# Optimization experiments

Hardware: AMD Instinct MI355X
Metric: run time of the kernel (lower is better)

## Reference

```python
import jax, jax.numpy as jnp
import numpy as np

D = 1024   # hidden_size
H = 16     # n_head
K = 64     # head_size
B = 4
T = 1024
LAYER_ID = 12
NUM_LAYERS = 24
D_MIX = 32
D_DECAY = 64


def setup_inputs() -> dict:
    key = jax.random.key(0)
    ks = jax.random.split(key, 12)
    r01 = LAYER_ID / (NUM_LAYERS - 1)          # ratio_0_to_1
    r10 = 1.0 - LAYER_ID / NUM_LAYERS          # ratio_1_to_almost0
    ddd = jnp.arange(D, dtype=jnp.float32) / D
    maa = lambda p: (1.0 - ddd ** p).reshape(1, 1, D)
    inp = {}
    inp['x'] = jax.random.normal(ks[0], (B, T, D), jnp.float32)
    inp['time_maa_x'] = maa(r10)
    inp['time_maa_w'] = maa(r10)
    inp['time_maa_k'] = maa(r10)
    inp['time_maa_v'] = (1.0 - (ddd ** r10 + 0.3 * r01)).reshape(1, 1, D)
    inp['time_maa_r'] = maa(0.5 * r10)
    inp['time_maa_g'] = maa(0.5 * r10)
    # torch inits time_maa_w1 to zeros (trivial); use small uniform like w2 for a non-degenerate test
    inp['time_maa_w1'] = jax.random.uniform(ks[1], (D, D_MIX * 5), jnp.float32, -0.01, 0.01)
    inp['time_maa_w2'] = jax.random.uniform(ks[2], (5, D_MIX, D), jnp.float32, -0.01, 0.01)
    n = jnp.arange(D, dtype=jnp.float32)
    inp['time_decay'] = (-6.0 + 5.0 * (n / (D - 1)) ** (0.7 + 1.3 * r01)).reshape(1, 1, D)
    inp['time_decay_w1'] = jax.random.uniform(ks[3], (D, D_DECAY), jnp.float32, -0.01, 0.01)
    inp['time_decay_w2'] = jax.random.uniform(ks[4], (D_DECAY, D), jnp.float32, -0.01, 0.01)
    for nm, kk in zip(['W_r', 'W_k', 'W_v', 'W_g', 'W_o'], ks[5:10]):
        inp[nm] = jax.random.normal(kk, (D, D), jnp.float32) * 0.02
    inp['ln_w'] = jnp.ones((D,), jnp.float32)
    inp['ln_b'] = jnp.zeros((D,), jnp.float32)
    return inp


def _bidir_shift(x):
    # (x[i-1] + x[i+1]) / 2 with zero padding at the boundaries
    left = jnp.pad(x[:, :-1, :], ((0, 0), (1, 0), (0, 0)))
    right = jnp.pad(x[:, 1:, :], ((0, 0), (0, 1), (0, 0)))
    return 0.5 * (left + right)


def _lion_attention(r, k, v, w):
    # r,k,v,w: (B,H,T,Khd), w = -exp(decay) <= 0
    Tn = r.shape[2]
    cs = jnp.cumsum(w, axis=2)
    cs_b = cs - w
    shift_f = cs[:, :, Tn // 2:Tn // 2 + 1, :]
    shift_b = cs_b[:, :, Tn // 2:Tn // 2 + 1, :]
    cf = jnp.clip(cs - shift_f, -60.0, 60.0)
    cb = jnp.clip(cs_b - shift_b, -60.0, 60.0)
    # A_fwd = tril(Q*e^{cf} @ (K*e^{-cf})^T); A_bwd = triu(Q*e^{-cb} @ (K*e^{cb})^T, 1)
    A_f = jnp.einsum('bhik,bhjk->bhij', r * jnp.exp(cf), k * jnp.exp(-cf))
    A_b = jnp.einsum('bhik,bhjk->bhij', r * jnp.exp(-cb), k * jnp.exp(cb))
    idx = jnp.arange(Tn)
    lower = idx[:, None] >= idx[None, :]   # tril incl. diagonal
    A = jnp.where(lower, A_f, A_b)         # == tril(A_f) + triu(A_b, 1)
    return jnp.einsum('bhij,bhjk->bhik', A, v)


def reference(x, time_maa_x, time_maa_w, time_maa_k, time_maa_v, time_maa_r, time_maa_g,
              time_maa_w1, time_maa_w2, time_decay, time_decay_w1, time_decay_w2,
              W_r, W_k, W_v, W_g, W_o, ln_w, ln_b):
    Bn, Tn, Dn = x.shape
    Hh, Kk = H, Dn // H
    dxprev = _bidir_shift(x) - x
    # data-dependent token-shift mixing coefficients (LoRA-style)
    xxx = jnp.tanh((x + dxprev * time_maa_x) @ time_maa_w1)          # (B,T,5*32)
    mm = jnp.einsum('btfm,fmd->fbtd', xxx.reshape(Bn, Tn, 5, D_MIX), time_maa_w2)
    mw, mk, mv, mr, mg = mm[0], mm[1], mm[2], mm[3], mm[4]
    xw = x + dxprev * (time_maa_w + mw)
    xk = x + dxprev * (time_maa_k + mk)
    xv = x + dxprev * (time_maa_v + mv)
    xr = x + dxprev * (time_maa_r + mr)
    xg = x + dxprev * (time_maa_g + mg)
    r = xr @ W_r.T
    k = xk @ W_k.T
    v = xv @ W_v.T
    g = jax.nn.silu(xg @ W_g.T)
    w = time_decay + jnp.tanh(xw @ time_decay_w1) @ time_decay_w2   # (B,T,D)
    to_h = lambda t: t.reshape(Bn, Tn, Hh, Kk).transpose(0, 2, 1, 3)
    y = _lion_attention(to_h(r), to_h(k), to_h(v), -jnp.exp(to_h(w)))
    y = y.transpose(0, 2, 1, 3).reshape(Bn * Tn, Dn)
    # GroupNorm(n_head groups, eps = 1e-5 * head_size_divisor^2)
    eps = 1e-5 * 64.0
    yg = y.reshape(Bn * Tn, Hh, Kk)
    mu = jnp.mean(yg, axis=-1, keepdims=True)
    var = jnp.var(yg, axis=-1, keepdims=True)
    yn = ((yg - mu) * jax.lax.rsqrt(var + eps)).reshape(Bn * Tn, Dn) * ln_w + ln_b
    y = yn.reshape(Bn, Tn, Dn)
    return (y * g) @ W_o.T
```

## Files before the change

kernel.cpp:

```cpp
#include <hip/hip_runtime.h>
#include <math.h>

#define NB 4
#define TT 1024
#define DD 1024
#define NTOK 4096
#define ND (NTOK*DD)

typedef __attribute__((ext_vector_type(8))) short bh8;
typedef __attribute__((ext_vector_type(4))) float fx4;

__device__ __forceinline__ unsigned short f2bf(float f) {
    unsigned int b = __float_as_uint(f);
    b += 0x7fffu + ((b >> 16) & 1u);
    return (unsigned short)(b >> 16);
}

__device__ __forceinline__ unsigned pkbf(float a, float b) {
#if __has_builtin(__builtin_amdgcn_cvt_pk_bf16_f32)
    auto r = __builtin_amdgcn_cvt_pk_bf16_f32(a, b);
    unsigned u;
    __builtin_memcpy(&u, &r, 4);
    return u;
#else
    return ((unsigned)f2bf(b) << 16) | f2bf(a);
#endif
}

#define GLD16(gp, lp) __builtin_amdgcn_global_load_lds( \
    (__attribute__((address_space(1))) void*)(gp), \
    (__attribute__((address_space(3))) void*)(lp), 16, 0, 0)

#define BARF() do { __builtin_amdgcn_s_barrier(); asm volatile("" ::: "memory"); } while (0)

__global__ __launch_bounds__(256) void k_prep(const float* __restrict__ W_r, const float* __restrict__ W_k,
                                              const float* __restrict__ W_v, const float* __restrict__ W_g,
                                              const float* __restrict__ W_o,
                                              const float* __restrict__ w1, const float* __restrict__ dw1,
                                              const float* __restrict__ w2,
                                              unsigned short* __restrict__ Wrb, unsigned short* __restrict__ Wkb,
                                              unsigned short* __restrict__ Wvb, unsigned short* __restrict__ Wgb,
                                              unsigned short* __restrict__ Wob,
                                              unsigned short* __restrict__ w1T, unsigned short* __restrict__ dw1T,
                                              unsigned short* __restrict__ w2T16) {
    int y = blockIdx.y, bx = blockIdx.x, tid = threadIdx.x;
    if (y < 5) {
        if (bx >= 512) return;
        const float* s = (y == 0) ? W_r : (y == 1) ? W_k : (y == 2) ? W_v : (y == 3) ? W_g : W_o;
        unsigned short* d = (y == 0) ? Wrb : (y == 1) ? Wkb : (y == 2) ? Wvb : (y == 3) ? Wgb : Wob;
        int i = (bx * 256 + tid) * 8;
        float4 a = *(const float4*)(s + i);
        float4 b = *(const float4*)(s + i + 4);
        uint4 o;
        o.x = pkbf(a.x, a.y);
        o.y = pkbf(a.z, a.w);
        o.z = pkbf(b.x, b.y);
        o.w = pkbf(b.z, b.w);
        *(uint4*)(d + i) = o;
    } else if (y == 5) {
        int o = bx * 256 + tid;
        int r = o & 1023, c = o >> 10;
        w1T[o] = f2bf(w1[r * 160 + c]);
    } else {
        if (bx < 256) {
            int o = bx * 256 + tid;
            int r = o & 1023, c = o >> 10;
            dw1T[o] = f2bf(dw1[r * 64 + c]);
        } else if (bx < 276) {
            int wi = bx - 256;
            int f = wi >> 2;
            int d = (wi & 3) * 256 + tid;
#pragma unroll 8
            for (int m = 0; m < 32; m++)
                w2T16[(size_t)(f * 1024 + d) * 32 + m] = f2bf(w2[(size_t)(f * 32 + m) * 1024 + d]);
        }
    }
}

__global__ __launch_bounds__(256) void k_mixx(const float* __restrict__ x,
                                              const float* __restrict__ maa_x,
                                              unsigned short* __restrict__ xmix16) {
    int base = (blockIdx.x * 256 + threadIdx.x) * 4;
    int t = (base >> 10) & 1023;
    int d = base & 1023;
    float4 xv = *(const float4*)(x + base);
    float4 xm = (t > 0)    ? *(const float4*)(x + base - 1024) : make_float4(0, 0, 0, 0);
    float4 xp = (t < 1023) ? *(const float4*)(x + base + 1024) : make_float4(0, 0, 0, 0);
    float4 ma = *(const float4*)(maa_x + d);
    uint2 o;
    float a0 = xv.x + (0.5f * (xm.x + xp.x) - xv.x) * ma.x;
    float a1 = xv.y + (0.5f * (xm.y + xp.y) - xv.y) * ma.y;
    float a2 = xv.z + (0.5f * (xm.z + xp.z) - xv.z) * ma.z;
    float a3 = xv.w + (0.5f * (xm.w + xp.w) - xv.w) * ma.w;
    o.x = pkbf(a0, a1);
    o.y = pkbf(a2, a3);
    *(uint2*)(xmix16 + base) = o;
}

__global__ __launch_bounds__(64) void k_xxx2(const unsigned short* __restrict__ xmix16,
                                             const unsigned short* __restrict__ w1T,
                                             unsigned short* __restrict__ xxx16) {
    int lane = threadIdx.x;
    int l15 = lane & 15, qd = lane >> 4;
    int m0 = blockIdx.x * 16;
    fx4 acc[10];
#pragma unroll
    for (int nt = 0; nt < 10; nt++)
#pragma unroll
        for (int r = 0; r < 4; r++) acc[nt][r] = 0.f;
#pragma unroll 2
    for (int kb = 0; kb < 1024; kb += 32) {
        bh8 af = *(const bh8*)(xmix16 + (size_t)(m0 + l15) * 1024 + kb + qd * 8);
#pragma unroll
        for (int nt = 0; nt < 10; nt++) {
            bh8 bf = *(const bh8*)(w1T + (size_t)(nt * 16 + l15) * 1024 + kb + qd * 8);
            acc[nt] = __builtin_amdgcn_mfma_f32_16x16x32_bf16(af, bf, acc[nt], 0, 0, 0);
        }
    }
#pragma unroll
    for (int nt = 0; nt < 10; nt++)
#pragma unroll
        for (int r = 0; r < 4; r++)
            xxx16[(size_t)(m0 + qd * 4 + r) * 160 + nt * 16 + l15] = f2bf(tanhf(acc[nt][r]));
}

__global__ __launch_bounds__(256, 2) void k_mmix(const float* __restrict__ x,
                                                 const unsigned short* __restrict__ xxx16,
                                                 const unsigned short* __restrict__ w2T16,
                                                 const float* __restrict__ maa_w,
                                                 const float* __restrict__ maa_k,
                                                 const float* __restrict__ maa_v,
                                                 const float* __restrict__ maa_r,
                                                 const float* __restrict__ maa_g,
                                                 unsigned short* __restrict__ xw16,
                                                 unsigned short* __restrict__ xk16,
                                                 unsigned short* __restrict__ xv16,
                                                 unsigned short* __restrict__ xr16,
                                                 unsigned short* __restrict__ xg16) {
    int tid = threadIdx.x;
    int w = tid >> 6, lane = tid & 63, l15 = lane & 15, qd = lane >> 4;
    int n0 = blockIdx.x * 64;
    int m0w = blockIdx.y * 128 + w * 32;
    const float* maap[5] = {maa_w, maa_k, maa_v, maa_r, maa_g};
    unsigned short* outp[5] = {xw16, xk16, xv16, xr16, xg16};
    float xin[8][4], dxv[8][4];
#pragma unroll
    for (int mi = 0; mi < 2; mi++)
#pragma unroll
        for (int r = 0; r < 4; r++) {
            int tok = m0w + mi * 16 + qd * 4 + r;
            int t = tok & 1023;
#pragma unroll
            for (int ni = 0; ni < 4; ni++) {
                int d = n0 + ni * 16 + l15;
                size_t idx = (size_t)tok * 1024 + d;
                float xv = x[idx];
                float xm1 = (t > 0)    ? x[idx - 1024] : 0.f;
                float xp1 = (t < 1023) ? x[idx + 1024] : 0.f;
                xin[mi * 4 + r][ni] = xv;
                dxv[mi * 4 + r][ni] = 0.5f * (xm1 + xp1) - xv;
            }
        }
#pragma unroll
    for (int f = 0; f < 5; f++) {
        bh8 af[2], bf[4];
#pragma unroll
        for (int mi = 0; mi < 2; mi++)
            af[mi] = *(const bh8*)(xxx16 + (size_t)(m0w + mi * 16 + l15) * 160 + f * 32 + qd * 8);
#pragma unroll
        for (int ni = 0; ni < 4; ni++)
            bf[ni] = *(const bh8*)(w2T16 + (size_t)(f * 1024 + n0 + ni * 16 + l15) * 32 + qd * 8);
        fx4 acc[2][4];
#pragma unroll
        for (int mi = 0; mi < 2; mi++)
#pragma unroll
            for (int ni = 0; ni < 4; ni++) {
#pragma unroll
                for (int r = 0; r < 4; r++) acc[mi][ni][r] = 0.f;
                acc[mi][ni] = __builtin_amdgcn_mfma_f32_16x16x32_bf16(af[mi], bf[ni], acc[mi][ni], 0, 0, 0);
            }
        const float* maa = maap[f];
        unsigned short* op = outp[f];
#pragma unroll
        for (int ni = 0; ni < 4; ni++) {
            float mv = maa[n0 + ni * 16 + l15];
#pragma unroll
            for (int mi = 0; mi < 2; mi++)
#pragma unroll
                for (int r = 0; r < 4; r++) {
                    float o = xin[mi * 4 + r][ni] + dxv[mi * 4 + r][ni] * (mv + acc[mi][ni][r]);
                    op[(size_t)(m0w + mi * 16 + qd * 4 + r) * 1024 + n0 + ni * 16 + l15] = f2bf(o);
                }
        }
    }
}

__global__ __launch_bounds__(64) void k_dec1m(const unsigned short* __restrict__ xw16,
                                              const unsigned short* __restrict__ dw1T,
                                              float* __restrict__ dech) {
    int lane = threadIdx.x;
    int l15 = lane & 15, qd = lane >> 4;
    int m0 = blockIdx.x * 16;
    fx4 acc[4];
#pragma unroll
    for (int nt = 0; nt < 4; nt++)
#pragma unroll
        for (int r = 0; r < 4; r++) acc[nt][r] = 0.f;
#pragma unroll 2
    for (int kb = 0; kb < 1024; kb += 32) {
        bh8 af = *(const bh8*)(xw16 + (size_t)(m0 + l15) * 1024 + kb + qd * 8);
#pragma unroll
        for (int nt = 0; nt < 4; nt++) {
            bh8 bf = *(const bh8*)(dw1T + (size_t)(nt * 16 + l15) * 1024 + kb + qd * 8);
            acc[nt] = __builtin_amdgcn_mfma_f32_16x16x32_bf16(af, bf, acc[nt], 0, 0, 0);
        }
    }
#pragma unroll
    for (int nt = 0; nt < 4; nt++)
#pragma unroll
        for (int r = 0; r < 4; r++)
            dech[(size_t)(m0 + qd * 4 + r) * 64 + nt * 16 + l15] = tanhf(acc[nt][r]);
}

__global__ __launch_bounds__(256) void k_dec2(const float* __restrict__ dech,
                                              const float* __restrict__ dw2,
                                              const float* __restrict__ tdec,
                                              float* __restrict__ ew) {
    __shared__ float hl[8][64];
    int tid = threadIdx.x;
    int tok0 = blockIdx.x * 8;
    {
        int l = tid;        hl[l >> 6][l & 63] = dech[tok0 * 64 + l];
        l = tid + 256;      hl[l >> 6][l & 63] = dech[tok0 * 64 + l];
    }
    __syncthreads();
#pragma unroll 1
    for (int c = 0; c < 4; c++) {
        int d = c * 256 + tid;
        float acc[8] = {};
#pragma unroll 8
        for (int j = 0; j < 64; j++) {
            float wv = dw2[j * 1024 + d];
#pragma unroll
            for (int g = 0; g < 8; g++) acc[g] = fmaf(hl[g][j], wv, acc[g]);
        }
        float td = tdec[d];
#pragma unroll
        for (int g = 0; g < 8; g++) ew[(tok0 + g) * 1024 + d] = -expf(td + acc[g]);
    }
}

__global__ __launch_bounds__(64) void k_scan1(const float* __restrict__ ew, float* __restrict__ segsum) {
    int bx = blockIdx.x;
    int b = bx >> 9, seg = (bx >> 4) & 31, dch = bx & 15;
    int d = dch * 64 + threadIdx.x;
    size_t base = ((size_t)(b * 1024 + seg * 32)) * 1024 + d;
    float s = 0.f;
#pragma unroll 8
    for (int t = 0; t < 32; t++) s += ew[base + (size_t)t * 1024];
    segsum[(b * 32 + seg) * 1024 + d] = s;
}

__global__ __launch_bounds__(64) void k_scan3(const float* __restrict__ ew, const float* __restrict__ segsum,
                                              float* __restrict__ cf, float* __restrict__ cb) {
    int bx = blockIdx.x;
    int b = bx >> 9, seg = (bx >> 4) & 31, dch = bx & 15;
    int d = dch * 64 + threadIdx.x;
    float run = 0.f, pre = 0.f, off16 = 0.f;
#pragma unroll
    for (int s = 0; s < 32; s++) {
        float tv = segsum[(b * 32 + s) * 1024 + d];
        if (s == seg) pre = run;
        if (s == 16) off16 = run;
        run += tv;
    }
    float e512 = ew[((size_t)(b * 1024 + 512)) * 1024 + d];
    float sb = off16;
    float sf = off16 + e512;
    float cum = pre;
    size_t base = ((size_t)(b * 1024 + seg * 32)) * 1024 + d;
#pragma unroll 4
    for (int t = 0; t < 32; t++) {
        float prev = cum;
        cum += ew[base + (size_t)t * 1024];
        cf[base + (size_t)t * 1024] = fminf(fmaxf(cum - sf, -60.f), 60.f);
        cb[base + (size_t)t * 1024] = fminf(fmaxf(prev - sb, -60.f), 60.f);
    }
}

template<int NW, int BNv>
__device__ __forceinline__ void gemm_v5(const unsigned short* __restrict__ A,
                                        const unsigned short* __restrict__ W,
                                        int m0, int n0, int mode,
                                        float* __restrict__ Cf,
                                        unsigned short* __restrict__ O1,
                                        unsigned short* __restrict__ O2,
                                        const float* __restrict__ cfp,
                                        const float* __restrict__ cbp,
                                        char* smem) {
    constexpr int AR = 128 / NW;
    constexpr int AG = AR / 16;
    constexpr int BR = BNv / NW;
    constexpr int BG = BR / 16;
    constexpr int LPW = AG + BG;
    constexpr int SLOT = (128 + BNv) * 64;
    constexpr int WNC = BNv / 64;

    int tid = threadIdx.x;
    int lane = tid & 63, w = tid >> 6;
    int l15 = lane & 15, qd = lane >> 4;
    int wm = w / WNC, wn = w % WNC;
    int lr = lane >> 2, lb = lane & 3;
    int gblk = lb ^ ((lr >> 1) & 3);
    const unsigned short* aSrc = A + (size_t)(m0 + w * AR + lr) * 1024 + gblk * 8;
    const unsigned short* bSrc = W + (size_t)(n0 + w * BR + lr) * 1024 + gblk * 8;
    int rc = (qd ^ ((l15 >> 1) & 3)) * 8;
    int arow = (wm * 64 + l15) * 32 + rc;
    int brow = (wn * 64 + l15) * 32 + rc;

    auto stage = [&](int off, int kbv) {
        unsigned short* _sa = (unsigned short*)(smem + off);
        unsigned short* _sb = _sa + 128 * 32;
#pragma unroll
        for (int i = 0; i < AG; ++i)
            GLD16(aSrc + kbv + (size_t)i * 16 * 1024, _sa + (w * AR + i * 16) * 32);
#pragma unroll
        for (int i = 0; i < BG; ++i)
            GLD16(bSrc + kbv + (size_t)i * 16 * 1024, _sb + (w * BR + i * 16) * 32);
    };

    fx4 acc[4][4];
#pragma unroll
    for (int mt = 0; mt < 4; mt++)
#pragma unroll
        for (int nt = 0; nt < 4; nt++)
#pragma unroll
            for (int r = 0; r < 4; r++) acc[mt][nt][r] = 0.f;

    stage(0, 0);
    stage(SLOT, 32);
    if constexpr (LPW == 3) asm volatile("s_waitcnt vmcnt(3)" ::: "memory");
    else                    asm volatile("s_waitcnt vmcnt(4)" ::: "memory");
    BARF();

    int oc = 0, on = SLOT, o2 = 2 * SLOT;
#pragma unroll 1
    for (int t = 0; t < 32; ++t) {
        if (t < 30) stage(o2, (t + 2) * 32);
        const unsigned short* cA = (const unsigned short*)(smem + oc);
        const unsigned short* cB = cA + 128 * 32;
        bh8 a[4], b[4];
#pragma unroll
        for (int mt = 0; mt < 4; ++mt) a[mt] = *(const bh8*)(cA + arow + mt * 512);
#pragma unroll
        for (int nt = 0; nt < 4; ++nt) b[nt] = *(const bh8*)(cB + brow + nt * 512);
        __builtin_amdgcn_s_setprio(1);
#pragma unroll
        for (int nt = 0; nt < 4; ++nt)
#pragma unroll
            for (int mt = 0; mt < 4; ++mt)
                acc[mt][nt] = __builtin_amdgcn_mfma_f32_16x16x32_bf16(a[mt], b[nt], acc[mt][nt], 0, 0, 0);
        __builtin_amdgcn_s_setprio(0);
        asm volatile("s_waitcnt lgkmcnt(0)" ::: "memory");
        if (t < 30) {
            if constexpr (LPW == 3) asm volatile("s_waitcnt vmcnt(3)" ::: "memory");
            else                    asm volatile("s_waitcnt vmcnt(4)" ::: "memory");
        } else if (t == 30) {
            asm volatile("s_waitcnt vmcnt(0)" ::: "memory");
        }
        BARF();
        int tmp = oc; oc = on; on = o2; o2 = tmp;
    }

    int mb = m0 + wm * 64, nb = n0 + wn * 64;
    if (mode <= 1) {
#pragma unroll
        for (int mt = 0; mt < 4; mt++)
#pragma unroll
            for (int nt = 0; nt < 4; nt++)
#pragma unroll
                for (int r = 0; r < 4; r++) {
                    float v = acc[mt][nt][r];
                    if (mode == 1) v = v / (1.f + __expf(-v));
                    Cf[(size_t)(mb + mt * 16 + qd * 4 + r) * 1024 + nb + nt * 16 + l15] = v;
                }
    } else if (mode <= 3) {
        float s1 = (mode == 2) ? 1.f : -1.f;
#pragma unroll
        for (int mt = 0; mt < 4; mt++)
#pragma unroll
            for (int nt = 0; nt < 4; nt++)
#pragma unroll
                for (int r = 0; r < 4; r++) {
                    size_t idx = (size_t)(mb + mt * 16 + qd * 4 + r) * 1024 + nb + nt * 16 + l15;
                    float v = acc[mt][nt][r];
                    O1[idx] = f2bf(v * __expf(s1 * cfp[idx]));
                    O2[idx] = f2bf(v * __expf(-s1 * cbp[idx]));
                }
    } else {
        unsigned short* T = (unsigned short*)smem;
        int bq = m0 >> 10, t0 = m0 & 1023;
#pragma unroll
        for (int mt = 0; mt < 4; mt++)
#pragma unroll
            for (int nt = 0; nt < 4; nt++) {
                int dl = wn * 64 + nt * 16 + l15;
                int tl = wm * 64 + mt * 16 + qd * 4;
                uint2 pk2;
                pk2.x = pkbf(acc[mt][nt][0], acc[mt][nt][1]);
                pk2.y = pkbf(acc[mt][nt][2], acc[mt][nt][3]);
                *(uint2*)(T + dl * 136 + tl) = pk2;
            }
        asm volatile("s_waitcnt lgkmcnt(0)" ::: "memory");
        BARF();
#pragma unroll
        for (int p = 0; p < 8; ++p) {
            int idx = p * (NW * 64) + tid;
            int dd = idx >> 4, u = idx & 15;
            uint4 vv = *(const uint4*)(T + dd * 136 + u * 8);
            *(uint4*)(O1 + (size_t)(bq * 1024 + n0 + dd) * 1024 + t0 + u * 8) = vv;
        }
    }
}

__global__ __launch_bounds__(512, 4) void k_qkvg(const unsigned short* __restrict__ xr16,
                                                 const unsigned short* __restrict__ xk16,
                                                 const unsigned short* __restrict__ xv16,
                                                 const unsigned short* __restrict__ xg16,
                                                 const unsigned short* __restrict__ Wrb,
                                                 const unsigned short* __restrict__ Wkb,
                                                 const unsigned short* __restrict__ Wvb,
                                                 const unsigned short* __restrict__ Wgb,
                                                 unsigned short* __restrict__ qf, unsigned short* __restrict__ qb,
                                                 unsigned short* __restrict__ kf, unsigned short* __restrict__ kb,
                                                 unsigned short* __restrict__ vvt,
                                                 float* __restrict__ gg,
                                                 const float* __restrict__ cf, const float* __restrict__ cb) {
    __shared__ __align__(16) char smem[73728];
    int flat = blockIdx.x;
    int wkid = (flat & 7) * 64 + (flat >> 3);
    int gy = wkid >> 7;
    int rem = wkid & 127;
    int m0 = (rem >> 2) * 128, n0 = (rem & 3) * 256;
    const unsigned short* Ap = (gy == 0) ? xr16 : (gy == 1) ? xk16 : (gy == 2) ? xv16 : xg16;
    const unsigned short* Wp = (gy == 0) ? Wrb : (gy == 1) ? Wkb : (gy == 2) ? Wvb : Wgb;
    int mode = (gy == 0) ? 2 : (gy == 1) ? 3 : (gy == 2) ? 4 : 1;
    unsigned short* o1 = (gy == 0) ? qf : (gy == 1) ? kf : (gy == 2) ? vvt : nullptr;
    unsigned short* o2 = (gy == 0) ? qb : (gy == 1) ? kb : nullptr;
    float* cfo = (gy == 3) ? gg : nullptr;
    gemm_v5<8, 256>(Ap, Wp, m0, n0, mode, cfo, o1, o2, cf, cb, smem);
}

__global__ __launch_bounds__(256, 3) void k_gemmo(const unsigned short* __restrict__ z16,
                                                  const unsigned short* __restrict__ Wob,
                                                  float* __restrict__ out) {
    __shared__ __align__(16) char smem[49152];
    int flat = blockIdx.x;
    int wkid = (flat & 7) * 32 + (flat >> 3);
    int m0 = (wkid >> 3) * 128, n0 = (wkid & 7) * 128;
    gemm_v5<4, 128>(z16, Wob, m0, n0, 0, out, nullptr, nullptr, nullptr, nullptr, smem);
}

__global__ __launch_bounds__(256, 2) void k_attn(const unsigned short* __restrict__ qf,
                                                 const unsigned short* __restrict__ qb,
                                                 const unsigned short* __restrict__ kf,
                                                 const unsigned short* __restrict__ kb,
                                                 const unsigned short* __restrict__ vvt,
                                                 float* __restrict__ y) {
    __shared__ __align__(16) char smem[32768];
    unsigned short* sK = (unsigned short*)smem;
    unsigned short* sV = (unsigned short*)(smem + 16384);
    int tid = threadIdx.x;
    int w = tid >> 6, lane = tid & 63, l15 = lane & 15, qd = lane >> 4;
    int bid = blockIdx.x;
    int bh = (bid & 7) + ((bid >> 6) << 3);
    int ib = (bid >> 3) & 7;
    int b = bh >> 4, h = bh & 15;
    int i0w = ib * 128 + w * 32;
    int bt0 = b * 1024;
    const unsigned short* vrow = vvt + (size_t)(b * 1024 + h * 64 + w * 16 + l15) * 1024 + qd * 8;
    int fmax = (i0w + 31) >> 6;
    int bmin = i0w >> 6;
    int srcA = l15 + ((lane & 16) << 1);
    int srcB = srcA + 16;
    fx4 yacc[4][2];
#pragma unroll
    for (int mt = 0; mt < 4; mt++)
#pragma unroll
        for (int nt = 0; nt < 2; nt++)
#pragma unroll
            for (int r = 0; r < 4; r++) yacc[mt][nt][r] = 0.f;

    for (int phase = 0; phase < 2; phase++) {
        const unsigned short* Q = phase ? qb : qf;
        const unsigned short* K = phase ? kb : kf;
        bh8 qfr[2][2];
#pragma unroll
        for (int nt = 0; nt < 2; nt++)
#pragma unroll
            for (int ks = 0; ks < 2; ks++)
                qfr[nt][ks] = *(const bh8*)(Q + (size_t)(bt0 + i0w + nt * 16 + l15) * 1024
                                              + h * 64 + ks * 32 + qd * 8);
        int jlo = phase == 0 ? 0 : 2 * ib;
        int jhi = phase == 0 ? 2 * ib + 1 : 15;
        const unsigned short* krow = K + (size_t)(bt0 + w * 16 + l15) * 1024 + h * 64 + qd * 8;
        for (int jt2 = jlo; jt2 <= jhi; jt2 += 2) {
            __syncthreads();
#pragma unroll
            for (int u = 0; u < 2; ++u) {
                size_t jb = (size_t)(jt2 + u) * 64;
                GLD16(krow + jb * 1024,        sK + u * 4096 + w * 512);
                GLD16(krow + jb * 1024 + 32,   sK + u * 4096 + 2048 + w * 512);
                GLD16(vrow + jb,               sV + u * 4096 + w * 512);
                GLD16(vrow + jb + 32,          sV + u * 4096 + 2048 + w * 512);
            }
            __syncthreads();
#pragma unroll
            for (int u = 0; u < 2; ++u) {
                int jt = jt2 + u;
                int jb = jt * 64;
                const unsigned short* bK = sK + u * 4096;
                const unsigned short* bV = sV + u * 4096;
                bool active = (phase == 0) ? (jt <= fmax) : (jt >= bmin);
                if (!active) continue;
                bool needmask = (phase == 0) ? (jb + 63 > i0w) : (i0w + 31 >= jb);
                bh8 kc[8];
#pragma unroll
                for (int fi = 0; fi < 8; fi++)
                    kc[fi] = *(const bh8*)(bK + fi * 512 + lane * 8);
                fx4 sacc[4][2];
#pragma unroll
                for (int mt = 0; mt < 4; mt++)
#pragma unroll
                    for (int nt = 0; nt < 2; nt++)
#pragma unroll
                        for (int r = 0; r < 4; r++) sacc[mt][nt][r] = 0.f;
#pragma unroll
                for (int ks = 0; ks < 2; ks++)
#pragma unroll
                    for (int mt = 0; mt < 4; mt++)
#pragma unroll
                        for (int nt = 0; nt < 2; nt++)
                            sacc[mt][nt] = __builtin_amdgcn_mfma_f32_16x16x32_bf16(kc[ks * 4 + mt], qfr[nt][ks], sacc[mt][nt], 0, 0, 0);
                uint2 pk[4][2];
#pragma unroll
                for (int mt = 0; mt < 4; mt++)
#pragma unroll
                    for (int nt = 0; nt < 2; nt++) {
                        fx4 s = sacc[mt][nt];
                        if (needmask) {
                            int ii = i0w + nt * 16 + l15;
                            int jj0 = jb + mt * 16 + qd * 4;
#pragma unroll
                            for (int r = 0; r < 4; r++) {
                                bool keep = (phase == 0) ? (ii >= jj0 + r) : (ii < jj0 + r);
                                if (!keep) s[r] = 0.f;
                            }
                        }
                        pk[mt][nt].x = pkbf(s[0], s[1]);
                        pk[mt][nt].y = pkbf(s[2], s[3]);
                    }
                bh8 vc[8];
#pragma unroll
                for (int fi = 0; fi < 8; fi++)
                    vc[fi] = *(const bh8*)(bV + fi * 512 + lane * 8);
#pragma unroll
                for (int ks2 = 0; ks2 < 2; ks2++) {
#pragma unroll
                    for (int nt = 0; nt < 2; nt++) {
                        int lox  = __shfl((int)pk[2 * ks2][nt].x,     srcA);
                        int hix  = __shfl((int)pk[2 * ks2 + 1][nt].x, srcA);
                        int loy  = __shfl((int)pk[2 * ks2][nt].y,     srcA);
                        int hiy  = __shfl((int)pk[2 * ks2 + 1][nt].y, srcA);
                        int lox2 = __shfl((int)pk[2 * ks2][nt].x,     srcB);
                        int hix2 = __shfl((int)pk[2 * ks2 + 1][nt].x, srcB);
                        int loy2 = __shfl((int)pk[2 * ks2][nt].y,     srcB);
                        int hiy2 = __shfl((int)pk[2 * ks2 + 1][nt].y, srcB);
                        union { int4 i; bh8 h; } cv;
                        cv.i.x = (qd & 2) ? hix  : lox;
                        cv.i.y = (qd & 2) ? hiy  : loy;
                        cv.i.z = (qd & 2) ? hix2 : lox2;
                        cv.i.w = (qd & 2) ? hiy2 : loy2;
#pragma unroll
                        for (int mt = 0; mt < 4; mt++)
                            yacc[mt][nt] = __builtin_amdgcn_mfma_f32_16x16x32_bf16(vc[ks2 * 4 + mt], cv.h, yacc[mt][nt], 0, 0, 0);
                    }
                }
            }
        }
    }
#pragma unroll
    for (int mt = 0; mt < 4; mt++)
#pragma unroll
        for (int nt = 0; nt < 2; nt++) {
            fx4 s = yacc[mt][nt];
            float4 o; o.x = s[0]; o.y = s[1]; o.z = s[2]; o.w = s[3];
            *(float4*)&y[(size_t)(bt0 + i0w + nt * 16 + l15) * 1024 + h * 64 + mt * 16 + qd * 4] = o;
        }
}

__global__ __launch_bounds__(256) void k_gn(const float* __restrict__ y,
                                            const float* __restrict__ g,
                                            const float* __restrict__ lnw,
                                            const float* __restrict__ lnb,
                                            unsigned short* __restrict__ z16) {
    int tid = threadIdx.x;
    int lane = tid & 63;
    int wv = tid >> 6;
    int group = blockIdx.x * 4 + wv;
    int tok = group >> 4, h = group & 15;
    int d = h * 64 + lane;
    size_t idx = (size_t)tok * 1024 + d;
    float val = y[idx];
    float s = val, s2 = val * val;
#pragma unroll
    for (int off = 32; off > 0; off >>= 1) {
        s  += __shfl_xor(s, off, 64);
        s2 += __shfl_xor(s2, off, 64);
    }
    float mu = s * (1.f / 64.f);
    float var = s2 * (1.f / 64.f) - mu * mu;
    float inv = rsqrtf(var + 6.4e-4f);
    float yn = (val - mu) * inv * lnw[d] + lnb[d];
    z16[idx] = f2bf(yn * g[idx]);
}

extern "C" void kernel_launch(void* const* d_in, const int* in_sizes, int n_in,
                              void* d_out, int out_size, void* d_ws, size_t ws_size,
                              hipStream_t stream) {
    const float* x     = (const float*)d_in[0];
    const float* maa_x = (const float*)d_in[1];
    const float* maa_w = (const float*)d_in[2];
    const float* maa_k = (const float*)d_in[3];
    const float* maa_v = (const float*)d_in[4];
    const float* maa_r = (const float*)d_in[5];
    const float* maa_g = (const float*)d_in[6];
    const float* w1    = (const float*)d_in[7];
    const float* w2    = (const float*)d_in[8];
    const float* tdec  = (const float*)d_in[9];
    const float* dw1   = (const float*)d_in[10];
    const float* dw2   = (const float*)d_in[11];
    const float* W_r   = (const float*)d_in[12];
    const float* W_k   = (const float*)d_in[13];
    const float* W_v   = (const float*)d_in[14];
    const float* W_g   = (const float*)d_in[15];
    const float* W_o   = (const float*)d_in[16];
    const float* lnw   = (const float*)d_in[17];
    const float* lnb   = (const float*)d_in[18];

    float* ws = (float*)d_ws;
    size_t o = 0;
    float* dech   = ws + o; o += 262144;
    float* segsum = ws + o; o += 131072;
    float* ew     = ws + o; o += 4194304;
    float* cf     = ws + o; o += 4194304;
    float* cb     = ws + o; o += 4194304;
    float* gg     = ws + o; o += 4194304;
    unsigned short* us = (unsigned short*)(ws + o);
    size_t u = 0;
    unsigned short* xmix16 = us + u; u += 4194304;
    unsigned short* xw16 = us + u; u += 4194304;
    unsigned short* xr16 = us + u; u += 4194304;
    unsigned short* xk16 = us + u; u += 4194304;
    unsigned short* xv16 = us + u; u += 4194304;
    unsigned short* xg16 = us + u; u += 4194304;
    unsigned short* qf   = us + u; u += 4194304;
    unsigned short* qb   = us + u; u += 4194304;
    unsigned short* kf   = us + u; u += 4194304;
    unsigned short* kb   = us + u; u += 4194304;
    unsigned short* vvt  = us + u; u += 4194304;
    unsigned short* Wrb  = us + u; u += 1048576;
    unsigned short* Wkb  = us + u; u += 1048576;
    unsigned short* Wvb  = us + u; u += 1048576;
    unsigned short* Wgb  = us + u; u += 1048576;
    unsigned short* Wob  = us + u; u += 1048576;
    unsigned short* w1T  = us + u; u += 163840;
    unsigned short* dw1T = us + u; u += 65536;
    unsigned short* xxx16 = us + u; u += 655360;
    unsigned short* w2T16 = us + u; u += 163840;
    float* yb0 = cf;
    unsigned short* z16 = xr16;

    k_prep<<<dim3(640, 7), 256, 0, stream>>>(W_r, W_k, W_v, W_g, W_o, w1, dw1, w2,
                                             Wrb, Wkb, Wvb, Wgb, Wob, w1T, dw1T, w2T16);
    k_mixx<<<4096, 256, 0, stream>>>(x, maa_x, xmix16);
    k_xxx2<<<256, 64, 0, stream>>>(xmix16, w1T, xxx16);
    k_mmix<<<dim3(16, 32), 256, 0, stream>>>(x, xxx16, w2T16, maa_w, maa_k, maa_v, maa_r, maa_g,
                                             xw16, xk16, xv16, xr16, xg16);
    k_dec1m<<<256, 64, 0, stream>>>(xw16, dw1T, dech);
    k_dec2<<<512, 256, 0, stream>>>(dech, dw2, tdec, ew);
    k_scan1<<<2048, 64, 0, stream>>>(ew, segsum);
    k_scan3<<<2048, 64, 0, stream>>>(ew, segsum, cf, cb);
    k_qkvg<<<dim3(512), dim3(512), 0, stream>>>(xr16, xk16, xv16, xg16, Wrb, Wkb, Wvb, Wgb,
                                                qf, qb, kf, kb, vvt, gg, cf, cb);
    k_attn<<<512, 256, 0, stream>>>(qf, qb, kf, kb, vvt, yb0);
    k_gn<<<16384, 256, 0, stream>>>(yb0, gg, lnw, lnb, z16);
    k_gemmo<<<256, 256, 0, stream>>>(z16, Wob, (float*)d_out);
}
```

Measured before the change: 321.6 us.

## Split-K the two skinny LoRA GEMMs across four waves and precompute dx

```diff
diff --git a/kernel.cpp b/kernel.cpp
--- a/kernel.cpp
+++ b/kernel.cpp
@@ -79,7 +79,8 @@
 
 __global__ __launch_bounds__(256) void k_mixx(const float* __restrict__ x,
                                               const float* __restrict__ maa_x,
-                                              unsigned short* __restrict__ xmix16) {
+                                              unsigned short* __restrict__ xmix16,
+                                              float* __restrict__ dxf) {
     int base = (blockIdx.x * 256 + threadIdx.x) * 4;
     int t = (base >> 10) & 1023;
     int d = base & 1023;
@@ -87,20 +88,24 @@
     float4 xm = (t > 0)    ? *(const float4*)(x + base - 1024) : make_float4(0, 0, 0, 0);
     float4 xp = (t < 1023) ? *(const float4*)(x + base + 1024) : make_float4(0, 0, 0, 0);
     float4 ma = *(const float4*)(maa_x + d);
+    float dx0 = 0.5f * (xm.x + xp.x) - xv.x;
+    float dx1 = 0.5f * (xm.y + xp.y) - xv.y;
+    float dx2 = 0.5f * (xm.z + xp.z) - xv.z;
+    float dx3 = 0.5f * (xm.w + xp.w) - xv.w;
     uint2 o;
-    float a0 = xv.x + (0.5f * (xm.x + xp.x) - xv.x) * ma.x;
-    float a1 = xv.y + (0.5f * (xm.y + xp.y) - xv.y) * ma.y;
-    float a2 = xv.z + (0.5f * (xm.z + xp.z) - xv.z) * ma.z;
-    float a3 = xv.w + (0.5f * (xm.w + xp.w) - xv.w) * ma.w;
-    o.x = pkbf(a0, a1);
-    o.y = pkbf(a2, a3);
+    o.x = pkbf(xv.x + dx0 * ma.x, xv.y + dx1 * ma.y);
+    o.y = pkbf(xv.z + dx2 * ma.z, xv.w + dx3 * ma.w);
     *(uint2*)(xmix16 + base) = o;
-}
-
-__global__ __launch_bounds__(64) void k_xxx2(const unsigned short* __restrict__ xmix16,
-                                             const unsigned short* __restrict__ w1T,
-                                             unsigned short* __restrict__ xxx16) {
-    int lane = threadIdx.x;
+    float4 dq; dq.x = dx0; dq.y = dx1; dq.z = dx2; dq.w = dx3;
+    *(float4*)(dxf + base) = dq;
+}
+
+__global__ __launch_bounds__(256) void k_xxx2(const unsigned short* __restrict__ xmix16,
+                                              const unsigned short* __restrict__ w1T,
+                                              unsigned short* __restrict__ xxx16) {
+    __shared__ __align__(16) float red[4][10][64][4];
+    int tid = threadIdx.x;
+    int lane = tid & 63, wv = tid >> 6;
     int l15 = lane & 15, qd = lane >> 4;
     int m0 = blockIdx.x * 16;
     fx4 acc[10];
@@ -108,8 +113,9 @@
     for (int nt = 0; nt < 10; nt++)
 #pragma unroll
         for (int r = 0; r < 4; r++) acc[nt][r] = 0.f;
+    int kb0 = wv * 256;
 #pragma unroll 2
-    for (int kb = 0; kb < 1024; kb += 32) {
+    for (int kb = kb0; kb < kb0 + 256; kb += 32) {
         bh8 af = *(const bh8*)(xmix16 + (size_t)(m0 + l15) * 1024 + kb + qd * 8);
 #pragma unroll
         for (int nt = 0; nt < 10; nt++) {
@@ -119,12 +125,24 @@
     }
 #pragma unroll
     for (int nt = 0; nt < 10; nt++)
-#pragma unroll
-        for (int r = 0; r < 4; r++)
-            xxx16[(size_t)(m0 + qd * 4 + r) * 160 + nt * 16 + l15] = f2bf(tanhf(acc[nt][r]));
+        *(fx4*)&red[wv][nt][lane][0] = acc[nt];
+    __syncthreads();
+    if (wv == 0) {
+#pragma unroll
+        for (int nt = 0; nt < 10; nt++) {
+            fx4 s = *(const fx4*)&red[0][nt][lane][0];
+            s = s + *(const fx4*)&red[1][nt][lane][0];
+            s = s + *(const fx4*)&red[2][nt][lane][0];
+            s = s + *(const fx4*)&red[3][nt][lane][0];
+#pragma unroll
+            for (int r = 0; r < 4; r++)
+                xxx16[(size_t)(m0 + qd * 4 + r) * 160 + nt * 16 + l15] = f2bf(tanhf(s[r]));
+        }
+    }
 }
 
 __global__ __launch_bounds__(256, 2) void k_mmix(const float* __restrict__ x,
+                                                 const float* __restrict__ dxf,
                                                  const unsigned short* __restrict__ xxx16,
                                                  const unsigned short* __restrict__ w2T16,
                                                  const float* __restrict__ maa_w,
@@ -149,16 +167,12 @@
 #pragma unroll
         for (int r = 0; r < 4; r++) {
             int tok = m0w + mi * 16 + qd * 4 + r;
-            int t = tok & 1023;
 #pragma unroll
             for (int ni = 0; ni < 4; ni++) {
                 int d = n0 + ni * 16 + l15;
                 size_t idx = (size_t)tok * 1024 + d;
-                float xv = x[idx];
-                float xm1 = (t > 0)    ? x[idx - 1024] : 0.f;
-                float xp1 = (t < 1023) ? x[idx + 1024] : 0.f;
-                xin[mi * 4 + r][ni] = xv;
-                dxv[mi * 4 + r][ni] = 0.5f * (xm1 + xp1) - xv;
+                xin[mi * 4 + r][ni] = x[idx];
+                dxv[mi * 4 + r][ni] = dxf[idx];
             }
         }
 #pragma unroll
@@ -195,10 +209,12 @@
     }
 }
 
-__global__ __launch_bounds__(64) void k_dec1m(const unsigned short* __restrict__ xw16,
-                                              const unsigned short* __restrict__ dw1T,
-                                              float* __restrict__ dech) {
-    int lane = threadIdx.x;
+__global__ __launch_bounds__(256) void k_dec1m(const unsigned short* __restrict__ xw16,
+                                               const unsigned short* __restrict__ dw1T,
+                                               float* __restrict__ dech) {
+    __shared__ __align__(16) float red[4][4][64][4];
+    int tid = threadIdx.x;
+    int lane = tid & 63, wv = tid >> 6;
     int l15 = lane & 15, qd = lane >> 4;
     int m0 = blockIdx.x * 16;
     fx4 acc[4];
@@ -206,8 +222,9 @@
     for (int nt = 0; nt < 4; nt++)
 #pragma unroll
         for (int r = 0; r < 4; r++) acc[nt][r] = 0.f;
+    int kb0 = wv * 256;
 #pragma unroll 2
-    for (int kb = 0; kb < 1024; kb += 32) {
+    for (int kb = kb0; kb < kb0 + 256; kb += 32) {
         bh8 af = *(const bh8*)(xw16 + (size_t)(m0 + l15) * 1024 + kb + qd * 8);
 #pragma unroll
         for (int nt = 0; nt < 4; nt++) {
@@ -217,9 +234,20 @@
     }
 #pragma unroll
     for (int nt = 0; nt < 4; nt++)
-#pragma unroll
-        for (int r = 0; r < 4; r++)
-            dech[(size_t)(m0 + qd * 4 + r) * 64 + nt * 16 + l15] = tanhf(acc[nt][r]);
+        *(fx4*)&red[wv][nt][lane][0] = acc[nt];
+    __syncthreads();
+    if (wv == 0) {
+#pragma unroll
+        for (int nt = 0; nt < 4; nt++) {
+            fx4 s = *(const fx4*)&red[0][nt][lane][0];
+            s = s + *(const fx4*)&red[1][nt][lane][0];
+            s = s + *(const fx4*)&red[2][nt][lane][0];
+            s = s + *(const fx4*)&red[3][nt][lane][0];
+#pragma unroll
+            for (int r = 0; r < 4; r++)
+                dech[(size_t)(m0 + qd * 4 + r) * 64 + nt * 16 + l15] = tanhf(s[r]);
+        }
+    }
 }
 
 __global__ __launch_bounds__(256) void k_dec2(const float* __restrict__ dech,
@@ -680,14 +708,15 @@
     unsigned short* w2T16 = us + u; u += 163840;
     float* yb0 = cf;
     unsigned short* z16 = xr16;
+    float* dxf = gg;
 
     k_prep<<<dim3(640, 7), 256, 0, stream>>>(W_r, W_k, W_v, W_g, W_o, w1, dw1, w2,
                                              Wrb, Wkb, Wvb, Wgb, Wob, w1T, dw1T, w2T16);
-    k_mixx<<<4096, 256, 0, stream>>>(x, maa_x, xmix16);
-    k_xxx2<<<256, 64, 0, stream>>>(xmix16, w1T, xxx16);
-    k_mmix<<<dim3(16, 32), 256, 0, stream>>>(x, xxx16, w2T16, maa_w, maa_k, maa_v, maa_r, maa_g,
+    k_mixx<<<4096, 256, 0, stream>>>(x, maa_x, xmix16, dxf);
+    k_xxx2<<<256, 256, 0, stream>>>(xmix16, w1T, xxx16);
+    k_mmix<<<dim3(16, 32), 256, 0, stream>>>(x, dxf, xxx16, w2T16, maa_w, maa_k, maa_v, maa_r, maa_g,
                                              xw16, xk16, xv16, xr16, xg16);
-    k_dec1m<<<256, 64, 0, stream>>>(xw16, dw1T, dech);
+    k_dec1m<<<256, 256, 0, stream>>>(xw16, dw1T, dech);
     k_dec2<<<512, 256, 0, stream>>>(dech, dw2, tdec, ew);
     k_scan1<<<2048, 64, 0, stream>>>(ew, segsum);
     k_scan3<<<2048, 64, 0, stream>>>(ew, segsum, cf, cb);
```

After: 338.0 us. +5.1%, slower.
